# Optimization experiments

Hardware: AMD Instinct MI355X
Metric: run time of the kernel (lower is better)

Reference implementation:

```python
import jax, jax.numpy as jnp
import numpy as np

H = 128  # hidden size

def lstm_layer(x, Wih, Whh, bih, bhh):
    """One PyTorch-semantics LSTM layer. x: (B,T,F). Gate order: i,f,g,o."""
    B = x.shape[0]
    # Precompute input contributions for all timesteps: (B,T,4H)
    xg = jnp.einsum('btf,gf->btg', x, Wih) + bih + bhh
    def step(carry, xt):
        h, c = carry
        g = xt + h @ Whh.T                      # (B,4H)
        i, f, gg, o = jnp.split(g, 4, axis=-1)
        i = jax.nn.sigmoid(i)
        f = jax.nn.sigmoid(f)
        gg = jnp.tanh(gg)
        o = jax.nn.sigmoid(o)
        c = f * c + i * gg
        h = o * jnp.tanh(c)
        return (h, c), h
    h0 = jnp.zeros((B, H), x.dtype)
    (hT, cT), hs = jax.lax.scan(step, (h0, h0), jnp.swapaxes(xg, 0, 1))
    return jnp.swapaxes(hs, 0, 1), hT  # (B,T,H), (B,H)


def setup_inputs() -> dict:
    key = jax.random.key(0)
    ks = jax.random.split(key, 20)
    B, T = 256, 2048
    s = 1.0 / np.sqrt(H)  # PyTorch default init scale
    inp = {
        'x': jax.random.normal(ks[0], (B, T, 1), jnp.float32),
        'Wih0': jax.random.uniform(ks[1], (4 * H, 1), jnp.float32, -s, s),
        'Whh0': jax.random.uniform(ks[2], (4 * H, H), jnp.float32, -s, s),
        'bih0': jax.random.uniform(ks[3], (4 * H,), jnp.float32, -s, s),
        'bhh0': jax.random.uniform(ks[4], (4 * H,), jnp.float32, -s, s),
        'Wih1': jax.random.uniform(ks[5], (4 * H, H), jnp.float32, -s, s),
        'Whh1': jax.random.uniform(ks[6], (4 * H, H), jnp.float32, -s, s),
        'bih1': jax.random.uniform(ks[7], (4 * H,), jnp.float32, -s, s),
        'bhh1': jax.random.uniform(ks[8], (4 * H,), jnp.float32, -s, s),
        'Wih2': jax.random.uniform(ks[9], (4 * H, H), jnp.float32, -s, s),
        'Whh2': jax.random.uniform(ks[10], (4 * H, H), jnp.float32, -s, s),
        'bih2': jax.random.uniform(ks[11], (4 * H,), jnp.float32, -s, s),
        'bhh2': jax.random.uniform(ks[12], (4 * H,), jnp.float32, -s, s),
        'fc1_w': jax.random.uniform(ks[13], (64, H), jnp.float32, -s, s),
        'fc1_b': jax.random.uniform(ks[14], (64,), jnp.float32, -s, s),
        'fc2_w': jax.random.uniform(ks[15], (5, 64), jnp.float32, -1.0 / 8, 1.0 / 8),
        'fc2_b': jax.random.uniform(ks[16], (5,), jnp.float32, -1.0 / 8, 1.0 / 8),
    }
    return inp


def reference(x, Wih0, Whh0, bih0, bhh0, Wih1, Whh1, bih1, bhh1,
              Wih2, Whh2, bih2, bhh2, fc1_w, fc1_b, fc2_w, fc2_b):
    # 3-layer LSTM (eval mode: inter-layer dropout is identity)
    h1, _ = lstm_layer(x, Wih0, Whh0, bih0, bhh0)
    h2, _ = lstm_layer(h1, Wih1, Whh1, bih1, bhh1)
    _, hT = lstm_layer(h2, Wih2, Whh2, bih2, bhh2)  # hn[-1]: (B,H)
    z = jax.nn.relu(hT @ fc1_w.T + fc1_b)
    return z @ fc2_w.T + fc2_b  # (B, num_classes)
```

## Files before the change

### kernel.cpp

```cpp
#include <hip/hip_runtime.h>


#define HDIM 128
#define TDIM 2048
#define BDIM 256
#define NT 512
#define XGP 20

typedef _Float16 half8_t __attribute__((ext_vector_type(8)));
typedef float f32x4 __attribute__((ext_vector_type(4)));

__device__ __forceinline__ f32x4 mfma16(half8_t a, half8_t b, f32x4 c) {
    return __builtin_amdgcn_mfma_f32_16x16x32_f16(a, b, c, 0, 0, 0);
}

__device__ __forceinline__ void fast_barrier() {
    asm volatile("s_waitcnt lgkmcnt(0)\n\ts_barrier" ::: "memory");
}

__global__ __launch_bounds__(256)
void convert_w(const float* __restrict__ Whh0, const float* __restrict__ Wih1,
               const float* __restrict__ Whh1, const float* __restrict__ Wih2,
               const float* __restrict__ Whh2, _Float16* __restrict__ dst) {
    int i = blockIdx.x * 256 + threadIdx.x;
    int seg = i >> 16, off = i & 65535;
    const float* s = (seg == 0) ? Whh0 : (seg == 1) ? Wih1 : (seg == 2) ? Whh1
                   : (seg == 3) ? Wih2 : Whh2;
    dst[i] = (_Float16)s[off];
}

#define RECG(Lc, A0_,A1_,A2_,A3_, selout_) { \
    f32x4 z0 = {0.f,0.f,0.f,0.f}; f32x4 z1 = z0, z2 = z0, z3 = z0; \
    z0 = mfma16(A0_, whf[Lc][0][0], z0); \
    z0 = mfma16(A1_, whf[Lc][0][1], z0); \
    z0 = mfma16(A2_, whf[Lc][0][2], z0); \
    z0 = mfma16(A3_, whf[Lc][0][3], z0); \
    z1 = mfma16(A0_, whf[Lc][1][0], z1); \
    z1 = mfma16(A1_, whf[Lc][1][1], z1); \
    z1 = mfma16(A2_, whf[Lc][1][2], z1); \
    z1 = mfma16(A3_, whf[Lc][1][3], z1); \
    z2 = mfma16(A0_, whf[Lc][2][0], z2); \
    z2 = mfma16(A1_, whf[Lc][2][1], z2); \
    z2 = mfma16(A2_, whf[Lc][2][2], z2); \
    z2 = mfma16(A3_, whf[Lc][2][3], z2); \
    z3 = mfma16(A0_, whf[Lc][3][0], z3); \
    z3 = mfma16(A1_, whf[Lc][3][1], z3); \
    z3 = mfma16(A2_, whf[Lc][3][2], z3); \
    z3 = mfma16(A3_, whf[Lc][3][3], z3); \
    float s0_ = qb1 ? z1[0] : z0[0]; \
    float s1_ = qb1 ? z3[0] : z2[0]; \
    selout_ = qb2 ? s1_ : s0_; }

#define GATECOMB(pre_, cr_, hout_) { \
    float e_ = __expf(me * (pre_)); \
    float r_ = __builtin_amdgcn_rcpf(1.0f + e_); \
    float a_ = fmaf(Bq, r_, Aq); \
    float v_ = __shfl_xor(a_, 32); \
    float p_ = a_ * v_;             \
    float f_ = __shfl_xor(a_, 16);  \
    float o_ = __shfl_xor(v_, 16);  \
    (cr_) = fmaf(f_, (cr_), p_); \
    float e2_ = __expf(2.0f * (cr_)); \
    float tc_ = fmaf(-2.0f, __builtin_amdgcn_rcpf(1.0f + e2_), 1.0f); \
    (hout_) = o_ * tc_; }

#define STEPL(Lc, RP_, WP_, PRE_) { \
    const _Float16* rp_ = (RP_); \
    half8_t A0_ = *(const half8_t*)(rp_ + kb); \
    half8_t A1_ = *(const half8_t*)(rp_ + 32 + kb); \
    half8_t A2_ = *(const half8_t*)(rp_ + 64 + kb); \
    half8_t A3_ = *(const half8_t*)(rp_ + 96 + kb); \
    float sel_; RECG(Lc, A0_,A1_,A2_,A3_, sel_); \
    float h_; GATECOMB((PRE_), cst[Lc], h_); \
    if (q == 0) (WP_)[wv*16 + n16] = (_Float16)h_; }

#define PROJ(XGI, HSRC, WIH) { \
    const _Float16* hr_ = &(HSRC)[n16][0]; \
    half8_t X0 = *(const half8_t*)(hr_ + kb); \
    half8_t X1 = *(const half8_t*)(hr_ + 32 + kb); \
    half8_t X2 = *(const half8_t*)(hr_ + 64 + kb); \
    half8_t X3 = *(const half8_t*)(hr_ + 96 + kb); \
    _Pragma("unroll") \
    for (int j = 0; j < 4; ++j) { \
      const int gp_ = (wv*4 + j)*16 + n16; \
      const _Float16* wp_ = (WIH) + (size_t)gp_*HDIM + kb; \
      half8_t B0 = *(const half8_t*)(wp_); \
      half8_t B1 = *(const half8_t*)(wp_ + 32); \
      half8_t B2 = *(const half8_t*)(wp_ + 64); \
      half8_t B3 = *(const half8_t*)(wp_ + 96); \
      f32x4 a_ = {0.f,0.f,0.f,0.f}; \
      a_ = mfma16(X0, B0, a_); a_ = mfma16(X1, B1, a_); \
      a_ = mfma16(X2, B2, a_); a_ = mfma16(X3, B3, a_); \
      *(f32x4*)&xg_s[XGI][gp_*XGP + q*4] = a_; \
    } }

__global__ __launch_bounds__(NT, 2)
void lstm3_kernel(const float* __restrict__ x,   const float* __restrict__ Wih0,
                  const float* __restrict__ bih0, const float* __restrict__ bhh0,
                  const float* __restrict__ bih1, const float* __restrict__ bhh1,
                  const float* __restrict__ bih2, const float* __restrict__ bhh2,
                  const float* __restrict__ fc1w, const float* __restrict__ fc1b,
                  const float* __restrict__ fc2w, const float* __restrict__ fc2b,
                  float* __restrict__ out, const _Float16* __restrict__ wbuf)
{
    __shared__ __align__(16) _Float16 hw[3][2][16][HDIM];
    __shared__ __align__(16) float xg_s[2][512 * XGP];
    __shared__ float x_s[16];
    __shared__ float z_s[64];

    const int tid = threadIdx.x;
    const int ln  = tid & 63;
    const int wv  = tid >> 6;
    const int n16 = ln & 15;
    const int q   = ln >> 4;
    const int kb  = q * 8;
    const bool qb1 = q & 1, qb2 = q & 2;
    const int b = blockIdx.x;

    { int* p = (int*)hw; for (int i = tid; i < 6144; i += NT) p[i] = 0; }

    half8_t whf[3][4][4];
    {
        const _Float16* wrec[3] = { wbuf, wbuf + (size_t)2*65536, wbuf + (size_t)4*65536 };
#pragma unroll
        for (int L = 0; L < 3; ++L)
#pragma unroll
            for (int tau = 0; tau < 4; ++tau)
#pragma unroll
                for (int kk = 0; kk < 4; ++kk)
                    whf[L][tau][kk] = *(const half8_t*)(wrec[L]
                        + (size_t)(tau*HDIM + wv*16 + n16)*HDIM + kk*32 + kb);
    }
    const _Float16* wih1p = wbuf + (size_t)1*65536;
    const _Float16* wih2p = wbuf + (size_t)3*65536;

    float bsv[3]; float w0v;
    {
        const float* bihs[3] = {bih0, bih1, bih2};
        const float* bhhs[3] = {bhh0, bhh1, bhh2};
        const int gate = q*HDIM + wv*16 + n16;
#pragma unroll
        for (int L = 0; L < 3; ++L) bsv[L] = bihs[L][gate] + bhhs[L][gate];
        w0v = Wih0[gate];
    }

    const float me = (q == 2) ? 2.0f : -1.0f;
    const float Aq = (q == 2) ? 1.0f : 0.0f;
    const float Bq = (q == 2) ? -2.0f : 1.0f;

    const int xgb = (q*HDIM + wv*16 + n16) * XGP;

    float cst[3] = {0.f, 0.f, 0.f};
    const float* xb = x + (size_t)b * TDIM;

#pragma unroll 1
    for (int s = 0; s < 130; ++s) {
        const int par = s & 1;
        const bool act0 = (s < 128), act1 = (s >= 1) && (s < 129), act2 = (s >= 2);

        fast_barrier();

        if (act0 && tid < 16) x_s[tid] = xb[s*16 + tid];
        if (act1) PROJ(0, hw[0][par^1], wih1p);
        if (act2) PROJ(1, hw[1][par], wih2p);

        fast_barrier();

#pragma unroll 1
        for (int tt = 0; tt < 16; ++tt) {
            if (tt) fast_barrier();
            const _Float16* r0p = tt ? hw[0][par][tt-1]   : hw[0][par^1][15];
            _Float16*       q0p = hw[0][par][tt];
            const _Float16* r1p = tt ? hw[1][par^1][tt-1] : hw[1][par][15];
            _Float16*       q1p = hw[1][par^1][tt];
            const _Float16* r2p = tt ? hw[2][par][tt-1]   : hw[2][par^1][15];
            _Float16*       q2p = hw[2][par][tt];
            const float xt = x_s[tt];

            if (act0 && act1 && act2) {
                STEPL(0, r0p, q0p, sel_ + fmaf(xt, w0v, bsv[0]));
                STEPL(1, r1p, q1p, sel_ + xg_s[0][xgb + tt] + bsv[1]);
                STEPL(2, r2p, q2p, sel_ + xg_s[1][xgb + tt] + bsv[2]);
            } else {
                if (act0) STEPL(0, r0p, q0p, sel_ + fmaf(xt, w0v, bsv[0]));
                if (act1) STEPL(1, r1p, q1p, sel_ + xg_s[0][xgb + tt] + bsv[1]);
                if (act2) STEPL(2, r2p, q2p, sel_ + xg_s[1][xgb + tt] + bsv[2]);
            }
        }
    }

    fast_barrier();
    if (tid < 64) {
        const float* w = fc1w + tid * HDIM;
        float sacc = fc1b[tid];
#pragma unroll
        for (int k = 0; k < HDIM; ++k) sacc += w[k] * (float)hw[2][1][15][k];
        z_s[tid] = fmaxf(sacc, 0.0f);
    }
    __syncthreads();
    if (tid < 5) {
        const float* w = fc2w + tid * 64;
        float sacc = fc2b[tid];
#pragma unroll
        for (int k = 0; k < 64; ++k) sacc += w[k] * z_s[k];
        out[b * 5 + tid] = sacc;
    }
}

extern "C" void kernel_launch(void* const* d_in, const int* in_sizes, int n_in,
                              void* d_out, int out_size, void* d_ws, size_t ws_size,
                              hipStream_t stream) {
    (void)in_sizes; (void)n_in; (void)out_size; (void)ws_size;
    const float* x    = (const float*)d_in[0];
    const float* Wih0 = (const float*)d_in[1];
    const float* Whh0 = (const float*)d_in[2];
    const float* bih0 = (const float*)d_in[3];
    const float* bhh0 = (const float*)d_in[4];
    const float* Wih1 = (const float*)d_in[5];
    const float* Whh1 = (const float*)d_in[6];
    const float* bih1 = (const float*)d_in[7];
    const float* bhh1 = (const float*)d_in[8];
    const float* Wih2 = (const float*)d_in[9];
    const float* Whh2 = (const float*)d_in[10];
    const float* bih2 = (const float*)d_in[11];
    const float* bhh2 = (const float*)d_in[12];
    const float* fc1w = (const float*)d_in[13];
    const float* fc1b = (const float*)d_in[14];
    const float* fc2w = (const float*)d_in[15];
    const float* fc2b = (const float*)d_in[16];
    float* out = (float*)d_out;

    _Float16* wbuf = (_Float16*)d_ws;

    hipLaunchKernelGGL(convert_w, dim3(1280), dim3(256), 0, stream,
                       Whh0, Wih1, Whh1, Wih2, Whh2, wbuf);
    hipLaunchKernelGGL(lstm3_kernel, dim3(BDIM), dim3(NT), 0, stream,
                       x, Wih0, bih0, bhh0, bih1, bhh1, bih2, bhh2,
                       fc1w, fc1b, fc2w, fc2b, out, wbuf);
}
```

Measured before the change: 3.542 ms.

## Pipeline LSTM layers across workgroups with batched sequences and global flag handoff

Replaces the one-sequence-per-block kernel, which ran all three layers in every block, with 48 blocks: each handles one layer for a group of 16 sequences. The recurrent matmul now uses the full MFMA M dimension (16 sequences) instead of wasting rows. Layers hand off 16-step chunks of hidden state through a global buffer, synchronised with acquire/release flags. Shared-memory h tiles use XOR swizzling. Only 48 of the GPU's CUs are used, and the design relies on producer and consumer blocks being resident at the same time.

```diff
diff --git a/kernel.cpp b/kernel.cpp
--- a/kernel.cpp
+++ b/kernel.cpp
@@ -3,9 +3,11 @@
 
 #define HDIM 128
 #define TDIM 2048
-#define BDIM 256
+#define NB 16
+#define NG 16
+#define CH 16
+#define NCH 128
 #define NT 512
-#define XGP 20
 
 typedef _Float16 half8_t __attribute__((ext_vector_type(8)));
 typedef float f32x4 __attribute__((ext_vector_type(4)));
@@ -16,194 +18,211 @@
 
 __device__ __forceinline__ void fast_barrier() {
     asm volatile("s_waitcnt lgkmcnt(0)\n\ts_barrier" ::: "memory");
+}
+
+__device__ __forceinline__ float sigm_f(float x) {
+    return __builtin_amdgcn_rcpf(1.0f + __expf(-x));
+}
+__device__ __forceinline__ float tanh_f(float x) {
+    return fmaf(-2.0f, __builtin_amdgcn_rcpf(1.0f + __expf(2.0f * x)), 1.0f);
 }
 
 __global__ __launch_bounds__(256)
 void convert_w(const float* __restrict__ Whh0, const float* __restrict__ Wih1,
                const float* __restrict__ Whh1, const float* __restrict__ Wih2,
-               const float* __restrict__ Whh2, _Float16* __restrict__ dst) {
+               const float* __restrict__ Whh2, _Float16* __restrict__ dst,
+               int* __restrict__ flags) {
     int i = blockIdx.x * 256 + threadIdx.x;
+    if (i < 2 * NG * NCH) flags[i] = 0;
     int seg = i >> 16, off = i & 65535;
     const float* s = (seg == 0) ? Whh0 : (seg == 1) ? Wih1 : (seg == 2) ? Whh1
                    : (seg == 3) ? Wih2 : Whh2;
     dst[i] = (_Float16)s[off];
 }
 
-#define RECG(Lc, A0_,A1_,A2_,A3_, selout_) { \
-    f32x4 z0 = {0.f,0.f,0.f,0.f}; f32x4 z1 = z0, z2 = z0, z3 = z0; \
-    z0 = mfma16(A0_, whf[Lc][0][0], z0); \
-    z0 = mfma16(A1_, whf[Lc][0][1], z0); \
-    z0 = mfma16(A2_, whf[Lc][0][2], z0); \
-    z0 = mfma16(A3_, whf[Lc][0][3], z0); \
-    z1 = mfma16(A0_, whf[Lc][1][0], z1); \
-    z1 = mfma16(A1_, whf[Lc][1][1], z1); \
-    z1 = mfma16(A2_, whf[Lc][1][2], z1); \
-    z1 = mfma16(A3_, whf[Lc][1][3], z1); \
-    z2 = mfma16(A0_, whf[Lc][2][0], z2); \
-    z2 = mfma16(A1_, whf[Lc][2][1], z2); \
-    z2 = mfma16(A2_, whf[Lc][2][2], z2); \
-    z2 = mfma16(A3_, whf[Lc][2][3], z2); \
-    z3 = mfma16(A0_, whf[Lc][3][0], z3); \
-    z3 = mfma16(A1_, whf[Lc][3][1], z3); \
-    z3 = mfma16(A2_, whf[Lc][3][2], z3); \
-    z3 = mfma16(A3_, whf[Lc][3][3], z3); \
-    float s0_ = qb1 ? z1[0] : z0[0]; \
-    float s1_ = qb1 ? z3[0] : z2[0]; \
-    selout_ = qb2 ? s1_ : s0_; }
-
-#define GATECOMB(pre_, cr_, hout_) { \
-    float e_ = __expf(me * (pre_)); \
-    float r_ = __builtin_amdgcn_rcpf(1.0f + e_); \
-    float a_ = fmaf(Bq, r_, Aq); \
-    float v_ = __shfl_xor(a_, 32); \
-    float p_ = a_ * v_;             \
-    float f_ = __shfl_xor(a_, 16);  \
-    float o_ = __shfl_xor(v_, 16);  \
-    (cr_) = fmaf(f_, (cr_), p_); \
-    float e2_ = __expf(2.0f * (cr_)); \
-    float tc_ = fmaf(-2.0f, __builtin_amdgcn_rcpf(1.0f + e2_), 1.0f); \
-    (hout_) = o_ * tc_; }
-
-#define STEPL(Lc, RP_, WP_, PRE_) { \
-    const _Float16* rp_ = (RP_); \
-    half8_t A0_ = *(const half8_t*)(rp_ + kb); \
-    half8_t A1_ = *(const half8_t*)(rp_ + 32 + kb); \
-    half8_t A2_ = *(const half8_t*)(rp_ + 64 + kb); \
-    half8_t A3_ = *(const half8_t*)(rp_ + 96 + kb); \
-    float sel_; RECG(Lc, A0_,A1_,A2_,A3_, sel_); \
-    float h_; GATECOMB((PRE_), cst[Lc], h_); \
-    if (q == 0) (WP_)[wv*16 + n16] = (_Float16)h_; }
-
-#define PROJ(XGI, HSRC, WIH) { \
-    const _Float16* hr_ = &(HSRC)[n16][0]; \
-    half8_t X0 = *(const half8_t*)(hr_ + kb); \
-    half8_t X1 = *(const half8_t*)(hr_ + 32 + kb); \
-    half8_t X2 = *(const half8_t*)(hr_ + 64 + kb); \
-    half8_t X3 = *(const half8_t*)(hr_ + 96 + kb); \
-    _Pragma("unroll") \
-    for (int j = 0; j < 4; ++j) { \
-      const int gp_ = (wv*4 + j)*16 + n16; \
-      const _Float16* wp_ = (WIH) + (size_t)gp_*HDIM + kb; \
-      half8_t B0 = *(const half8_t*)(wp_); \
-      half8_t B1 = *(const half8_t*)(wp_ + 32); \
-      half8_t B2 = *(const half8_t*)(wp_ + 64); \
-      half8_t B3 = *(const half8_t*)(wp_ + 96); \
-      f32x4 a_ = {0.f,0.f,0.f,0.f}; \
-      a_ = mfma16(X0, B0, a_); a_ = mfma16(X1, B1, a_); \
-      a_ = mfma16(X2, B2, a_); a_ = mfma16(X3, B3, a_); \
-      *(f32x4*)&xg_s[XGI][gp_*XGP + q*4] = a_; \
-    } }
-
 __global__ __launch_bounds__(NT, 2)
-void lstm3_kernel(const float* __restrict__ x,   const float* __restrict__ Wih0,
-                  const float* __restrict__ bih0, const float* __restrict__ bhh0,
-                  const float* __restrict__ bih1, const float* __restrict__ bhh1,
-                  const float* __restrict__ bih2, const float* __restrict__ bhh2,
-                  const float* __restrict__ fc1w, const float* __restrict__ fc1b,
-                  const float* __restrict__ fc2w, const float* __restrict__ fc2b,
-                  float* __restrict__ out, const _Float16* __restrict__ wbuf)
+void lstm3_pipe(const float* __restrict__ x,   const float* __restrict__ Wih0,
+                const float* __restrict__ bih0, const float* __restrict__ bhh0,
+                const float* __restrict__ bih1, const float* __restrict__ bhh1,
+                const float* __restrict__ bih2, const float* __restrict__ bhh2,
+                const float* __restrict__ fc1w, const float* __restrict__ fc1b,
+                const float* __restrict__ fc2w, const float* __restrict__ fc2b,
+                float* __restrict__ out,
+                _Float16* __restrict__ hbuf, const _Float16* __restrict__ wbuf,
+                int* __restrict__ flags)
 {
-    __shared__ __align__(16) _Float16 hw[3][2][16][HDIM];
-    __shared__ __align__(16) float xg_s[2][512 * XGP];
-    __shared__ float x_s[16];
-    __shared__ float z_s[64];
+    __shared__ __align__(16) _Float16 hown[CH * NB * HDIM];
+    __shared__ __align__(16) _Float16 hst [CH * NB * HDIM];
+    __shared__ float x_s[CH][NB];
+    __shared__ float z_s[NB][64];
+    __shared__ float hfin[NB][HDIM];
 
     const int tid = threadIdx.x;
-    const int ln  = tid & 63;
-    const int wv  = tid >> 6;
-    const int n16 = ln & 15;
-    const int q   = ln >> 4;
-    const int kb  = q * 8;
-    const bool qb1 = q & 1, qb2 = q & 2;
-    const int b = blockIdx.x;
-
-    { int* p = (int*)hw; for (int i = tid; i < 6144; i += NT) p[i] = 0; }
-
-    half8_t whf[3][4][4];
-    {
-        const _Float16* wrec[3] = { wbuf, wbuf + (size_t)2*65536, wbuf + (size_t)4*65536 };
-#pragma unroll
-        for (int L = 0; L < 3; ++L)
-#pragma unroll
-            for (int tau = 0; tau < 4; ++tau)
-#pragma unroll
-                for (int kk = 0; kk < 4; ++kk)
-                    whf[L][tau][kk] = *(const half8_t*)(wrec[L]
-                        + (size_t)(tau*HDIM + wv*16 + n16)*HDIM + kk*32 + kb);
-    }
-    const _Float16* wih1p = wbuf + (size_t)1*65536;
-    const _Float16* wih2p = wbuf + (size_t)3*65536;
-
-    float bsv[3]; float w0v;
-    {
-        const float* bihs[3] = {bih0, bih1, bih2};
-        const float* bhhs[3] = {bhh0, bhh1, bhh2};
-        const int gate = q*HDIM + wv*16 + n16;
-#pragma unroll
-        for (int L = 0; L < 3; ++L) bsv[L] = bihs[L][gate] + bhhs[L][gate];
-        w0v = Wih0[gate];
-    }
-
-    const float me = (q == 2) ? 2.0f : -1.0f;
-    const float Aq = (q == 2) ? 1.0f : 0.0f;
-    const float Bq = (q == 2) ? -2.0f : 1.0f;
-
-    const int xgb = (q*HDIM + wv*16 + n16) * XGP;
-
-    float cst[3] = {0.f, 0.f, 0.f};
-    const float* xb = x + (size_t)b * TDIM;
+    const int ln = tid & 63, wv = tid >> 6;
+    const int c = ln & 15, p = ln >> 4;
+    const int L = blockIdx.x >> 4;
+    const int g = blockIdx.x & 15;
+
+    const _Float16* whh = wbuf + (size_t)((L == 0) ? 0 : (L == 1) ? 2 : 4) * 65536;
+    const _Float16* wih = wbuf + (size_t)((L == 1) ? 1 : 3) * 65536;
+    half8_t whh_f[4][4], wih_f[4][4];
+#pragma unroll
+    for (int q = 0; q < 4; ++q)
+#pragma unroll
+        for (int m = 0; m < 4; ++m) {
+            whh_f[q][m] = *(const half8_t*)(whh + (size_t)(q*HDIM + wv*16 + c)*HDIM + m*32 + p*8);
+            if (L > 0)
+                wih_f[q][m] = *(const half8_t*)(wih + (size_t)(q*HDIM + wv*16 + c)*HDIM + m*32 + p*8);
+        }
+
+    const float* bihL = (L == 0) ? bih0 : (L == 1) ? bih1 : bih2;
+    const float* bhhL = (L == 0) ? bhh0 : (L == 1) ? bhh1 : bhh2;
+    const int u = wv * 16 + c;
+    float bias[4], w0[4];
+#pragma unroll
+    for (int q = 0; q < 4; ++q) {
+        bias[q] = bihL[q*HDIM + u] + bhhL[q*HDIM + u];
+        w0[q] = (L == 0) ? Wih0[q*HDIM + u] : 0.0f;
+    }
+
+    int roff[4], woff[4];
+#pragma unroll
+    for (int m = 0; m < 4; ++m)
+        roff[m] = c*HDIM + ((32*m + 8*p) ^ (8*(c & 7)));
+#pragma unroll
+    for (int r = 0; r < 4; ++r) {
+        int seq = p*4 + r;
+        woff[r] = seq*HDIM + (u ^ (8*(seq & 7)));
+    }
+
+    for (int i = tid; i < NB*HDIM/2; i += NT)
+        ((int*)(hown + 15*NB*HDIM))[i] = 0;
+    float cc[4] = {0.f, 0.f, 0.f, 0.f};
+    __syncthreads();
+
+    int* fprod = flags + (L*NG + g)*NCH;
+    int* fcons = flags + ((L-1)*NG + g)*NCH;
+    const float* xb = x + (size_t)(g*NB)*TDIM;
 
 #pragma unroll 1
-    for (int s = 0; s < 130; ++s) {
-        const int par = s & 1;
-        const bool act0 = (s < 128), act1 = (s >= 1) && (s < 129), act2 = (s >= 2);
-
+    for (int s = 0; s < NCH; ++s) {
+        _Float16* gch = hbuf + ((size_t)(g*NCH + s) << 15);
+
+        if (L == 0) {
+            if (tid < CH*NB)
+                x_s[tid >> 4][tid & 15] = xb[(size_t)(tid & 15)*TDIM + s*CH + (tid >> 4)];
+        } else {
+            if (tid == 0) {
+                while (__hip_atomic_load(fcons + s, __ATOMIC_ACQUIRE,
+                                         __HIP_MEMORY_SCOPE_AGENT) == 0)
+                    __builtin_amdgcn_s_sleep(8);
+            }
+            __syncthreads();
+            const float4* gsrc = (const float4*)gch;
+            float4* dv = (float4*)hst;
+#pragma unroll
+            for (int k2 = 0; k2 < 8; ++k2) dv[k2*NT + tid] = gsrc[k2*NT + tid];
+        }
         fast_barrier();
 
-        if (act0 && tid < 16) x_s[tid] = xb[s*16 + tid];
-        if (act1) PROJ(0, hw[0][par^1], wih1p);
-        if (act2) PROJ(1, hw[1][par], wih2p);
-
-        fast_barrier();
-
 #pragma unroll 1
-        for (int tt = 0; tt < 16; ++tt) {
-            if (tt) fast_barrier();
-            const _Float16* r0p = tt ? hw[0][par][tt-1]   : hw[0][par^1][15];
-            _Float16*       q0p = hw[0][par][tt];
-            const _Float16* r1p = tt ? hw[1][par^1][tt-1] : hw[1][par][15];
-            _Float16*       q1p = hw[1][par^1][tt];
-            const _Float16* r2p = tt ? hw[2][par][tt-1]   : hw[2][par^1][15];
-            _Float16*       q2p = hw[2][par][tt];
-            const float xt = x_s[tt];
-
-            if (act0 && act1 && act2) {
-                STEPL(0, r0p, q0p, sel_ + fmaf(xt, w0v, bsv[0]));
-                STEPL(1, r1p, q1p, sel_ + xg_s[0][xgb + tt] + bsv[1]);
-                STEPL(2, r2p, q2p, sel_ + xg_s[1][xgb + tt] + bsv[2]);
+        for (int tt = 0; tt < CH; ++tt) {
+            const int tp = (tt + CH - 1) & 15;
+            const _Float16* rsl = hown + tp*(NB*HDIM);
+            const _Float16* psl = hst  + tt*(NB*HDIM);
+            half8_t A0 = *(const half8_t*)(rsl + roff[0]);
+            half8_t A1 = *(const half8_t*)(rsl + roff[1]);
+            half8_t A2 = *(const half8_t*)(rsl + roff[2]);
+            half8_t A3 = *(const half8_t*)(rsl + roff[3]);
+
+            f32x4 acc[4];
+            if (L > 0) {
+                half8_t P0 = *(const half8_t*)(psl + roff[0]);
+                half8_t P1 = *(const half8_t*)(psl + roff[1]);
+                half8_t P2 = *(const half8_t*)(psl + roff[2]);
+                half8_t P3 = *(const half8_t*)(psl + roff[3]);
+#pragma unroll
+                for (int q = 0; q < 4; ++q) {
+                    f32x4 a = {0.f, 0.f, 0.f, 0.f};
+                    a = mfma16(P0, wih_f[q][0], a);
+                    a = mfma16(P1, wih_f[q][1], a);
+                    a = mfma16(P2, wih_f[q][2], a);
+                    a = mfma16(P3, wih_f[q][3], a);
+                    acc[q] = a;
+                }
             } else {
-                if (act0) STEPL(0, r0p, q0p, sel_ + fmaf(xt, w0v, bsv[0]));
-                if (act1) STEPL(1, r1p, q1p, sel_ + xg_s[0][xgb + tt] + bsv[1]);
-                if (act2) STEPL(2, r2p, q2p, sel_ + xg_s[1][xgb + tt] + bsv[2]);
-            }
-        }
-    }
-
-    fast_barrier();
-    if (tid < 64) {
-        const float* w = fc1w + tid * HDIM;
-        float sacc = fc1b[tid];
-#pragma unroll
-        for (int k = 0; k < HDIM; ++k) sacc += w[k] * (float)hw[2][1][15][k];
-        z_s[tid] = fmaxf(sacc, 0.0f);
-    }
-    __syncthreads();
-    if (tid < 5) {
-        const float* w = fc2w + tid * 64;
-        float sacc = fc2b[tid];
-#pragma unroll
-        for (int k = 0; k < 64; ++k) sacc += w[k] * z_s[k];
-        out[b * 5 + tid] = sacc;
+#pragma unroll
+                for (int q = 0; q < 4; ++q) acc[q] = (f32x4){0.f, 0.f, 0.f, 0.f};
+            }
+#pragma unroll
+            for (int q = 0; q < 4; ++q) {
+                acc[q] = mfma16(A0, whh_f[q][0], acc[q]);
+                acc[q] = mfma16(A1, whh_f[q][1], acc[q]);
+                acc[q] = mfma16(A2, whh_f[q][2], acc[q]);
+                acc[q] = mfma16(A3, whh_f[q][3], acc[q]);
+            }
+
+            _Float16* wsl = hown + tt*(NB*HDIM);
+#pragma unroll
+            for (int r = 0; r < 4; ++r) {
+                float pi = acc[0][r] + bias[0];
+                float pf = acc[1][r] + bias[1];
+                float pg = acc[2][r] + bias[2];
+                float po = acc[3][r] + bias[3];
+                if (L == 0) {
+                    float xr = x_s[tt][p*4 + r];
+                    pi = fmaf(xr, w0[0], pi); pf = fmaf(xr, w0[1], pf);
+                    pg = fmaf(xr, w0[2], pg); po = fmaf(xr, w0[3], po);
+                }
+                float ig = sigm_f(pi), fg = sigm_f(pf);
+                float gg = tanh_f(pg), og = sigm_f(po);
+                cc[r] = fmaf(fg, cc[r], ig * gg);
+                wsl[woff[r]] = (_Float16)(og * tanh_f(cc[r]));
+            }
+            fast_barrier();
+        }
+
+        if (L < 2) {
+            const float4* sv = (const float4*)hown;
+            float4* gdst = (float4*)gch;
+#pragma unroll
+            for (int k2 = 0; k2 < 8; ++k2) gdst[k2*NT + tid] = sv[k2*NT + tid];
+            __threadfence();
+            __syncthreads();
+            if (tid == 0)
+                __hip_atomic_store(fprod + s, 1, __ATOMIC_RELEASE,
+                                   __HIP_MEMORY_SCOPE_AGENT);
+        }
+    }
+
+    if (L == 2) {
+        __syncthreads();
+        for (int i = tid; i < NB*HDIM; i += NT) {
+            int seq = i >> 7, uu = i & 127;
+            hfin[seq][uu] = (float)hown[15*NB*HDIM + seq*HDIM + (uu ^ (8*(seq & 7)))];
+        }
+        __syncthreads();
+        for (int d = tid; d < NB*64; d += NT) {
+            int seq = d >> 6, un = d & 63;
+            const float4* w4 = (const float4*)(fc1w + un*HDIM);
+            const float4* h4 = (const float4*)hfin[seq];
+            float sacc = fc1b[un];
+#pragma unroll
+            for (int k2 = 0; k2 < 32; ++k2) {
+                float4 a = w4[k2], bb = h4[k2];
+                sacc += a.x*bb.x + a.y*bb.y + a.z*bb.z + a.w*bb.w;
+            }
+            z_s[seq][un] = fmaxf(sacc, 0.0f);
+        }
+        __syncthreads();
+        for (int d = tid; d < NB*5; d += NT) {
+            int seq = d / 5, o = d - seq*5;
+            const float* w = fc2w + o*64;
+            float sacc = fc2b[o];
+#pragma unroll
+            for (int k2 = 0; k2 < 64; ++k2) sacc += w[k2] * z_s[seq][k2];
+            out[(size_t)(g*NB + seq)*5 + o] = sacc;
+        }
     }
 }
 
@@ -230,11 +249,13 @@
     const float* fc2b = (const float*)d_in[16];
     float* out = (float*)d_out;
 
-    _Float16* wbuf = (_Float16*)d_ws;
+    _Float16* hbuf = (_Float16*)d_ws;
+    _Float16* wbuf = hbuf + (size_t)67108864;
+    int* flags = (int*)(wbuf + (size_t)5*65536);
 
     hipLaunchKernelGGL(convert_w, dim3(1280), dim3(256), 0, stream,
-                       Whh0, Wih1, Whh1, Wih2, Whh2, wbuf);
-    hipLaunchKernelGGL(lstm3_kernel, dim3(BDIM), dim3(NT), 0, stream,
+                       Whh0, Wih1, Whh1, Wih2, Whh2, wbuf, flags);
+    hipLaunchKernelGGL(lstm3_pipe, dim3(3*NG), dim3(NT), 0, stream,
                        x, Wih0, bih0, bhh0, bih1, bhh1, bih2, bhh2,
-                       fc1w, fc1b, fc2w, fc2b, out, wbuf);
-}
+                       fc1w, fc1b, fc2w, fc2b, out, hbuf, wbuf, flags);
+}
```

Result: slower. 3.733 ms (+5.4%).
